# Kernel optimization log

Hardware: AMD Instinct MI355X
Metric: run time of the kernel (lower is better)

## Reference

```python
import jax, jax.numpy as jnp
import numpy as np

DIAG = 64          # dynamic_mask_scale: |i-j| >= DIAG is masked
NEG_INF = float('-inf')

def _band_mask(L, diagonal):
    # True where masked out: j >= i + diagonal or i >= j + diagonal  <=>  |i-j| >= diagonal
    i = jnp.arange(L)[:, None]
    j = jnp.arange(L)[None, :]
    return jnp.abs(i - j) >= diagonal  # [L, L] bool

def setup_inputs() -> dict:
    key = jax.random.key(0)
    k1, k2, k3, k4 = jax.random.split(key, 4)
    B, L, H, E = 2, 2048, 8, 64
    queries = jax.random.normal(k1, (B, L, H, E), dtype=jnp.float32)
    keys = jax.random.normal(k2, (B, L, H, E), dtype=jnp.float32)
    values = jax.random.normal(k3, (B, L, H, E), dtype=jnp.float32)
    sigma = jax.random.normal(k4, (B, L, H), dtype=jnp.float32)
    attn_mask = jnp.zeros((B, 1, L, L), dtype=bool)  # unused (dynamic mask path)
    return {"queries": queries, "keys": keys, "values": values,
            "sigma": sigma, "attn_mask": attn_mask}

def reference(queries, keys, values, sigma, attn_mask):
    B, L, H, E = queries.shape
    scale = 1.0 / jnp.sqrt(jnp.float32(E))
    # scores: [B, H, L, S]
    scores = jnp.einsum('blhe,bshe->bhls', queries, keys)
    mask = _band_mask(L, DIAG)  # [L, L]
    scores = jnp.where(mask[None, None, :, :], NEG_INF, scores)
    attn = scale * scores
    series = jax.nn.softmax(attn, axis=-1)  # dropout p=0 -> identity
    V = jnp.einsum('bhls,bshd->blhd', series, values)
    return (V, series)
```

## Files before the change

### kernel.cpp

```cpp
#include <hip/hip_runtime.h>
#include <cstdint>

#define BB    2
#define LL    2048
#define HH    8
#define EE    64
#define DIAG  64
#define RR    16
#define WCAP  144
#define SKB   36
#define SQB   36
#define PS    148
#define NT    256

typedef __attribute__((ext_vector_type(8))) short bf16x8;
typedef __attribute__((ext_vector_type(4))) float f32x4;


__device__ __forceinline__ void nt_store4(const float4 v, float4* p) {
    __builtin_nontemporal_store(*(const f32x4*)&v, (f32x4*)p);
}

__global__ __launch_bounds__(NT, 4) void anomaly_attn_kernel(
    const float* __restrict__ Q,
    const float* __restrict__ K,
    const float* __restrict__ V,
    float* __restrict__ outV,
    float* __restrict__ outS)
{
    __shared__ unsigned lds_k[WCAP * SKB];
    __shared__ unsigned lds_qb[RR * SQB];
    __shared__ float    lds_sp[RR * PS];

    const int bid  = blockIdx.x;
    const int gblk = (bid & 7) * 256 + (bid >> 3);
    const int rb   = gblk & 127;
    const int h    = (gblk >> 7) & 7;
    const int b    = gblk >> 10;
    const int i0   = rb * RR;

    const int t    = threadIdx.x;
    const int wave = t >> 6;
    const int lane = t & 63;

    const size_t headOff = ((size_t)b * LL * HH + h) * EE;
    const int    rowStr  = HH * EE;

    const int j0  = i0 - 64;
    const int j04 = j0 >> 2;

    float* srow0 = outS + (((size_t)(b * HH + h)) * LL + i0) * LL;

    auto pack2 = [](float x, float y) -> unsigned {
        unsigned ux = __float_as_uint(x);
        unsigned uy = __float_as_uint(y);
        unsigned bx = (ux + 0x7FFFu + ((ux >> 16) & 1u)) >> 16;
        unsigned by = (uy + 0x7FFFu + ((uy >> 16) & 1u)) >> 16;
        return bx | (by << 16);
    };
    auto lo = [](unsigned u) -> float { return __uint_as_float(u << 16); };
    auto hi = [](unsigned u) -> float { return __uint_as_float(u & 0xFFFF0000u); };

    {
        const int qrow = t >> 4, qf = t & 15;
        const float4 qv = *(const float4*)(Q + headOff + (size_t)(i0 + qrow) * rowStr + qf * 4);
        uint2 qp; qp.x = pack2(qv.x, qv.y); qp.y = pack2(qv.z, qv.w);
        *(uint2*)(lds_qb + qrow * SQB + qf * 2) = qp;
        for (int idx = t; idx < WCAP * 16; idx += NT) {
            const int trow = idx >> 4, tf = idx & 15;
            int j = j0 + trow; j = j < 0 ? 0 : (j > LL - 1 ? LL - 1 : j);
            const float4 kv = *(const float4*)(K + headOff + (size_t)j * rowStr + tf * 4);
            uint2 pk; pk.x = pack2(kv.x, kv.y); pk.y = pack2(kv.z, kv.w);
            *(uint2*)(lds_k + trow * SKB + tf * 2) = pk;
        }
    }
    __syncthreads();

    {
        const int quad = lane >> 4;
        const int l16  = lane & 15;
        const bf16x8 a0 = *(const bf16x8*)(lds_qb + l16 * SQB + quad * 4);
        const bf16x8 a1 = *(const bf16x8*)(lds_qb + l16 * SQB + quad * 4 + 16);
        __builtin_amdgcn_s_setprio(1);
        for (int n = wave; n < 9; n += 4) {
            const unsigned* kb = lds_k + (16 * n + l16) * SKB + quad * 4;
            const bf16x8 b0 = *(const bf16x8*)(kb);
            const bf16x8 b1 = *(const bf16x8*)(kb + 16);
            f32x4 acc = {0.f, 0.f, 0.f, 0.f};
            acc = __builtin_amdgcn_mfma_f32_16x16x32_bf16(a0, b0, acc, 0, 0, 0);
            acc = __builtin_amdgcn_mfma_f32_16x16x32_bf16(a1, b1, acc, 0, 0, 0);
            float* dst = lds_sp + (quad * 4) * PS + 16 * n + l16;
            dst[0 * PS] = acc[0];
            dst[1 * PS] = acc[1];
            dst[2 * PS] = acc[2];
            dst[3 * PS] = acc[3];
        }
        __builtin_amdgcn_s_setprio(0);
    }
    __syncthreads();

    for (int idx = t; idx < WCAP * 16; idx += NT) {
        const int trow = idx >> 4, tf = idx & 15;
        int j = j0 + trow; j = j < 0 ? 0 : (j > LL - 1 ? LL - 1 : j);
        const float4 vv = *(const float4*)(V + headOff + (size_t)j * rowStr + tf * 4);
        uint2 pk; pk.x = pack2(vv.x, vv.y); pk.y = pack2(vv.z, vv.w);
        *(uint2*)(lds_k + trow * SKB + tf * 2) = pk;
    }

    const float scale = 0.125f;
    for (int r4 = 0; r4 < 4; ++r4) {
        const int r = wave * 4 + r4;
        float* sp = lds_sp + r * PS;
        const float x1 = sp[lane];
        const float x2 = sp[64 + lane];
        const float x3 = (lane < 16) ? sp[128 + lane] : 0.f;
        const bool v1 = (lane >= r + 1) && (j0 + lane >= 0);
        const bool v2 = (i0 + lane < LL);
        const bool v3 = (lane < 16) && (lane <= r - 1) && (i0 + 64 + lane < LL);
        float e1 = v1 ? x1 * scale : -3.0e38f;
        float e2 = v2 ? x2 * scale : -3.0e38f;
        float e3 = v3 ? x3 * scale : -3.0e38f;

        float m = fmaxf(e1, fmaxf(e2, e3));
#pragma unroll
        for (int off = 1; off < 64; off <<= 1)
            m = fmaxf(m, __shfl_xor(m, off, 64));
        float p1 = v1 ? __expf(e1 - m) : 0.f;
        float p2 = v2 ? __expf(e2 - m) : 0.f;
        float p3 = v3 ? __expf(e3 - m) : 0.f;
        float l = p1 + p2 + p3;
#pragma unroll
        for (int off = 1; off < 64; off <<= 1)
            l += __shfl_xor(l, off, 64);
        const float inv = 1.0f / l;
        sp[lane]      = p1 * inv;
        sp[64 + lane] = p2 * inv;
        if (lane < 16) sp[128 + lane] = p3 * inv;
    }

    {
        const int wstart4 = j04 < 0 ? 0 : j04;
        int wend4 = j04 + 36; if (wend4 > LL / 4) wend4 = LL / 4;
        for (int r4 = 0; r4 < 4; ++r4) {
            const int r = wave * 4 + r4;
            float4* srow4 = (float4*)(srow0 + (size_t)r * LL);
            const float4* sp4 = (const float4*)(lds_sp + r * PS);
#pragma unroll
            for (int k = 0; k < 8; ++k) {
                const int col4 = lane + k * 64;
                float4 v = make_float4(0.f, 0.f, 0.f, 0.f);
                if (col4 >= wstart4 && col4 < wend4)
                    v = sp4[col4 - j04];
                nt_store4(v, &srow4[col4]);
            }
        }
    }
    __syncthreads();

    {
        const int e4   = lane & 15;
        const int jsub = lane >> 4;
        const int rr0  = wave * 4;
        const float* pbase = lds_sp + rr0 * PS;
        float4 a0 = make_float4(0,0,0,0), a1 = a0, a2 = a0, a3 = a0;
        __builtin_amdgcn_s_setprio(1);
#pragma unroll
        for (int k = 0; k < WCAP / 4; ++k) {
            const int jrel = jsub + 4 * k;
            const uint2 pv = *(const uint2*)(lds_k + jrel * SKB + e4 * 2);
            const float v0 = lo(pv.x), v1 = hi(pv.x), v2 = lo(pv.y), v3 = hi(pv.y);
            const float w0 = pbase[jrel];
            const float w1 = pbase[PS + jrel];
            const float w2 = pbase[2 * PS + jrel];
            const float w3 = pbase[3 * PS + jrel];
            a0.x += w0 * v0; a0.y += w0 * v1; a0.z += w0 * v2; a0.w += w0 * v3;
            a1.x += w1 * v0; a1.y += w1 * v1; a1.z += w1 * v2; a1.w += w1 * v3;
            a2.x += w2 * v0; a2.y += w2 * v1; a2.z += w2 * v2; a2.w += w2 * v3;
            a3.x += w3 * v0; a3.y += w3 * v1; a3.z += w3 * v2; a3.w += w3 * v3;
        }
        __builtin_amdgcn_s_setprio(0);
#pragma unroll
        for (int off = 16; off <= 32; off <<= 1) {
            a0.x += __shfl_xor(a0.x, off, 64); a0.y += __shfl_xor(a0.y, off, 64);
            a0.z += __shfl_xor(a0.z, off, 64); a0.w += __shfl_xor(a0.w, off, 64);
            a1.x += __shfl_xor(a1.x, off, 64); a1.y += __shfl_xor(a1.y, off, 64);
            a1.z += __shfl_xor(a1.z, off, 64); a1.w += __shfl_xor(a1.w, off, 64);
            a2.x += __shfl_xor(a2.x, off, 64); a2.y += __shfl_xor(a2.y, off, 64);
            a2.z += __shfl_xor(a2.z, off, 64); a2.w += __shfl_xor(a2.w, off, 64);
            a3.x += __shfl_xor(a3.x, off, 64); a3.y += __shfl_xor(a3.y, off, 64);
            a3.z += __shfl_xor(a3.z, off, 64); a3.w += __shfl_xor(a3.w, off, 64);
        }
        if (lane < 16) {
            float4* o0 = (float4*)(outV + headOff + (size_t)(i0 + rr0 + 0) * rowStr);
            float4* o1 = (float4*)(outV + headOff + (size_t)(i0 + rr0 + 1) * rowStr);
            float4* o2 = (float4*)(outV + headOff + (size_t)(i0 + rr0 + 2) * rowStr);
            float4* o3 = (float4*)(outV + headOff + (size_t)(i0 + rr0 + 3) * rowStr);
            nt_store4(a0, &o0[e4]);
            nt_store4(a1, &o1[e4]);
            nt_store4(a2, &o2[e4]);
            nt_store4(a3, &o3[e4]);
        }
    }
}

extern "C" void kernel_launch(void* const* d_in, const int* in_sizes, int n_in,
                              void* d_out, int out_size, void* d_ws, size_t ws_size,
                              hipStream_t stream) {
    const float* Q = (const float*)d_in[0];
    const float* K = (const float*)d_in[1];
    const float* V = (const float*)d_in[2];

    float* outV = (float*)d_out;
    float* outS = (float*)d_out + (size_t)BB * LL * HH * EE;

    const int grid = (BB * HH * LL) / RR;
    anomaly_attn_kernel<<<grid, NT, 0, stream>>>(Q, K, V, outV, outS);
}
```

Measured before the change: 331.7 us.

## Compute P·V with bf16 MFMA using transposed V and bf16 probabilities in LDS

```diff
diff --git a/kernel.cpp b/kernel.cpp
--- a/kernel.cpp
+++ b/kernel.cpp
@@ -11,6 +11,8 @@
 #define SKB   36
 #define SQB   36
 #define PS    148
+#define PBS   168
+#define VTS   168
 #define NT    256
 
 typedef __attribute__((ext_vector_type(8))) short bf16x8;
@@ -28,9 +30,10 @@
     float* __restrict__ outV,
     float* __restrict__ outS)
 {
-    __shared__ unsigned lds_k[WCAP * SKB];
+    __shared__ unsigned lds_k[5376];
     __shared__ unsigned lds_qb[RR * SQB];
     __shared__ float    lds_sp[RR * PS];
+    __shared__ unsigned lds_pb[RR * (PBS/2)];
 
     const int bid  = blockIdx.x;
     const int gblk = (bid & 7) * 256 + (bid >> 3);
@@ -58,14 +61,20 @@
         unsigned by = (uy + 0x7FFFu + ((uy >> 16) & 1u)) >> 16;
         return bx | (by << 16);
     };
-    auto lo = [](unsigned u) -> float { return __uint_as_float(u << 16); };
-    auto hi = [](unsigned u) -> float { return __uint_as_float(u & 0xFFFF0000u); };
+    auto b16 = [](float x) -> unsigned short {
+        unsigned u = __float_as_uint(x);
+        return (unsigned short)((u + 0x7FFFu + ((u >> 16) & 1u)) >> 16);
+    };
 
     {
         const int qrow = t >> 4, qf = t & 15;
         const float4 qv = *(const float4*)(Q + headOff + (size_t)(i0 + qrow) * rowStr + qf * 4);
         uint2 qp; qp.x = pack2(qv.x, qv.y); qp.y = pack2(qv.z, qv.w);
         *(uint2*)(lds_qb + qrow * SQB + qf * 2) = qp;
+        if (t < 192) {
+            const int r = t / 12, d = t % 12;
+            lds_pb[r * (PBS/2) + 72 + d] = 0u;
+        }
         for (int idx = t; idx < WCAP * 16; idx += NT) {
             const int trow = idx >> 4, tf = idx & 15;
             int j = j0 + trow; j = j < 0 ? 0 : (j > LL - 1 ? LL - 1 : j);
@@ -99,15 +108,28 @@
     }
     __syncthreads();
 
-    for (int idx = t; idx < WCAP * 16; idx += NT) {
-        const int trow = idx >> 4, tf = idx & 15;
-        int j = j0 + trow; j = j < 0 ? 0 : (j > LL - 1 ? LL - 1 : j);
-        const float4 vv = *(const float4*)(V + headOff + (size_t)j * rowStr + tf * 4);
-        uint2 pk; pk.x = pack2(vv.x, vv.y); pk.y = pack2(vv.z, vv.w);
-        *(uint2*)(lds_k + trow * SKB + tf * 2) = pk;
+    {
+        unsigned* vt32 = lds_k;
+        for (int idx = t; idx < 512; idx += NT) {
+            const int e = idx >> 3, d = idx & 7;
+            vt32[e * (VTS/2) + 72 + d] = 0u;
+        }
+        for (int idx = t; idx < (WCAP/2) * 16; idx += NT) {
+            const int t2 = idx >> 4, tf = idx & 15;
+            int ja = j0 + 2 * t2;     ja = ja < 0 ? 0 : (ja > LL - 1 ? LL - 1 : ja);
+            int jb = j0 + 2 * t2 + 1; jb = jb < 0 ? 0 : (jb > LL - 1 ? LL - 1 : jb);
+            const float4 va = *(const float4*)(V + headOff + (size_t)ja * rowStr + tf * 4);
+            const float4 vb = *(const float4*)(V + headOff + (size_t)jb * rowStr + tf * 4);
+            unsigned* dst = vt32 + (tf * 4) * (VTS/2) + t2;
+            dst[0 * (VTS/2)] = pack2(va.x, vb.x);
+            dst[1 * (VTS/2)] = pack2(va.y, vb.y);
+            dst[2 * (VTS/2)] = pack2(va.z, vb.z);
+            dst[3 * (VTS/2)] = pack2(va.w, vb.w);
+        }
     }
 
     const float scale = 0.125f;
+    unsigned short* pb16 = (unsigned short*)lds_pb;
     for (int r4 = 0; r4 < 4; ++r4) {
         const int r = wave * 4 + r4;
         float* sp = lds_sp + r * PS;
@@ -133,9 +155,10 @@
         for (int off = 1; off < 64; off <<= 1)
             l += __shfl_xor(l, off, 64);
         const float inv = 1.0f / l;
-        sp[lane]      = p1 * inv;
-        sp[64 + lane] = p2 * inv;
-        if (lane < 16) sp[128 + lane] = p3 * inv;
+        const float q1 = p1 * inv, q2 = p2 * inv, q3 = p3 * inv;
+        sp[lane]      = q1;  pb16[r * PBS + lane]       = b16(q1);
+        sp[64 + lane] = q2;  pb16[r * PBS + 64 + lane]  = b16(q2);
+        if (lane < 16) { sp[128 + lane] = q3;  pb16[r * PBS + 128 + lane] = b16(q3); }
     }
 
     {
@@ -158,48 +181,23 @@
     __syncthreads();
 
     {
-        const int e4   = lane & 15;
-        const int jsub = lane >> 4;
-        const int rr0  = wave * 4;
-        const float* pbase = lds_sp + rr0 * PS;
-        float4 a0 = make_float4(0,0,0,0), a1 = a0, a2 = a0, a3 = a0;
+        const int l16  = lane & 15;
+        const int quad = lane >> 4;
+        const unsigned short* pbr  = pb16 + l16 * PBS;
+        const unsigned short* vrow = (const unsigned short*)lds_k + (wave * 16 + l16) * VTS;
+        f32x4 acc = {0.f, 0.f, 0.f, 0.f};
         __builtin_amdgcn_s_setprio(1);
 #pragma unroll
-        for (int k = 0; k < WCAP / 4; ++k) {
-            const int jrel = jsub + 4 * k;
-            const uint2 pv = *(const uint2*)(lds_k + jrel * SKB + e4 * 2);
-            const float v0 = lo(pv.x), v1 = hi(pv.x), v2 = lo(pv.y), v3 = hi(pv.y);
-            const float w0 = pbase[jrel];
-            const float w1 = pbase[PS + jrel];
-            const float w2 = pbase[2 * PS + jrel];
-            const float w3 = pbase[3 * PS + jrel];
-            a0.x += w0 * v0; a0.y += w0 * v1; a0.z += w0 * v2; a0.w += w0 * v3;
-            a1.x += w1 * v0; a1.y += w1 * v1; a1.z += w1 * v2; a1.w += w1 * v3;
-            a2.x += w2 * v0; a2.y += w2 * v1; a2.z += w2 * v2; a2.w += w2 * v3;
-            a3.x += w3 * v0; a3.y += w3 * v1; a3.z += w3 * v2; a3.w += w3 * v3;
+        for (int c = 0; c < 5; ++c) {
+            const bf16x8 a = *(const bf16x8*)(pbr  + c * 32 + quad * 8);
+            const bf16x8 v = *(const bf16x8*)(vrow + c * 32 + quad * 8);
+            acc = __builtin_amdgcn_mfma_f32_16x16x32_bf16(a, v, acc, 0, 0, 0);
         }
         __builtin_amdgcn_s_setprio(0);
-#pragma unroll
-        for (int off = 16; off <= 32; off <<= 1) {
-            a0.x += __shfl_xor(a0.x, off, 64); a0.y += __shfl_xor(a0.y, off, 64);
-            a0.z += __shfl_xor(a0.z, off, 64); a0.w += __shfl_xor(a0.w, off, 64);
-            a1.x += __shfl_xor(a1.x, off, 64); a1.y += __shfl_xor(a1.y, off, 64);
-            a1.z += __shfl_xor(a1.z, off, 64); a1.w += __shfl_xor(a1.w, off, 64);
-            a2.x += __shfl_xor(a2.x, off, 64); a2.y += __shfl_xor(a2.y, off, 64);
-            a2.z += __shfl_xor(a2.z, off, 64); a2.w += __shfl_xor(a2.w, off, 64);
-            a3.x += __shfl_xor(a3.x, off, 64); a3.y += __shfl_xor(a3.y, off, 64);
-            a3.z += __shfl_xor(a3.z, off, 64); a3.w += __shfl_xor(a3.w, off, 64);
-        }
-        if (lane < 16) {
-            float4* o0 = (float4*)(outV + headOff + (size_t)(i0 + rr0 + 0) * rowStr);
-            float4* o1 = (float4*)(outV + headOff + (size_t)(i0 + rr0 + 1) * rowStr);
-            float4* o2 = (float4*)(outV + headOff + (size_t)(i0 + rr0 + 2) * rowStr);
-            float4* o3 = (float4*)(outV + headOff + (size_t)(i0 + rr0 + 3) * rowStr);
-            nt_store4(a0, &o0[e4]);
-            nt_store4(a1, &o1[e4]);
-            nt_store4(a2, &o2[e4]);
-            nt_store4(a3, &o3[e4]);
-        }
+        float* o = outV + headOff + (size_t)(i0 + quad * 4) * rowStr + wave * 16 + l16;
+#pragma unroll
+        for (int r = 0; r < 4; ++r)
+            __builtin_nontemporal_store(acc[r], o + (size_t)r * rowStr);
     }
 }
 
```

Measured after the change: 325.1 us. 1.02x faster.
